# Performance work log

Hardware: AMD Instinct MI355X
Metric: run time of the kernel (lower is better)

The kernel has to match this reference:

```python
import jax, jax.numpy as jnp
import numpy as np

VOCAB = 32000
DIM = 1024
BATCH = 2
SEQ = 2048
CHUNK = 256
LCTX = 4            # local_context_size, mode='sum'
LOCAL_WIN = 512     # sparse_local_window (>= 2*chunk)
GSTRIDE = 1024      # sparse_global_stride (>= 4*chunk)
LN_EPS = 1e-5


def _cache_positions():
    """Simulate the deterministic sparse KV-cache pruning per chunk (numpy, trace-time).
    Returns list of key-position index arrays (cached positions ++ current chunk)."""
    cache = np.zeros((0,), dtype=np.int64)
    per_chunk = []
    for i in range(SEQ // CHUNK):
        new = np.arange(i * CHUNK, (i + 1) * CHUNK, dtype=np.int64)
        full = np.concatenate([cache, new])
        per_chunk.append(full)
        total_seen = (i + 1) * CHUNK
        local_start = max(0, total_seen - LOCAL_WIN)
        keep = (full >= local_start) | (full % GSTRIDE == 0)
        cache = full[keep]
    return per_chunk


def setup_inputs() -> dict:
    key = jax.random.key(0)
    ks = jax.random.split(key, 8)
    s = 0.02
    return {
        "x": jax.random.randint(ks[0], (BATCH, SEQ), 0, VOCAB, dtype=jnp.int64),
        "emb_table": jax.random.normal(ks[1], (VOCAB, DIM), jnp.float32) * s,
        "q_w": jax.random.normal(ks[2], (DIM, DIM), jnp.float32) * s,
        "q_b": jnp.zeros((DIM,), jnp.float32),
        "k_w": jax.random.normal(ks[3], (DIM, DIM), jnp.float32) * s,
        "k_b": jnp.zeros((DIM,), jnp.float32),
        "v_w": jax.random.normal(ks[4], (DIM, DIM), jnp.float32) * s,
        "v_b": jnp.zeros((DIM,), jnp.float32),
        "o_w": jax.random.normal(ks[5], (DIM, DIM), jnp.float32) * s,
        "o_b": jnp.zeros((DIM,), jnp.float32),
        "ln_w": jnp.ones((DIM,), jnp.float32),
        "ln_b": jnp.zeros((DIM,), jnp.float32),
        "out_w": jax.random.normal(ks[6], (VOCAB, DIM), jnp.float32) * s,
        "out_b": jnp.zeros((VOCAB,), jnp.float32),
    }


def reference(x, emb_table, q_w, q_b, k_w, k_b, v_w, v_b, o_w, o_b, ln_w, ln_b, out_w, out_b):
    # embedding + causal local context (sum of 0..LCTX-1 shifted embeddings)
    emb = emb_table[x]                                  # [B,S,D]
    ctx = emb
    for off in range(1, LCTX):
        ctx = ctx + jnp.pad(emb, ((0, 0), (off, 0), (0, 0)))[:, :SEQ]

    # project full sequence once (same per-chunk projections in the original)
    Q = ctx @ q_w.T + q_b                               # [B,S,D]
    K = ctx @ k_w.T + k_b
    V = ctx @ v_w.T + v_b
    scale = 1.0 / np.sqrt(DIM).astype(np.float32)

    outs = []
    for i, kpos in enumerate(_cache_positions()):
        qpos = np.arange(i * CHUNK, (i + 1) * CHUNK, dtype=np.int64)
        q = Q[:, i * CHUNK:(i + 1) * CHUNK]             # [B,C,D]
        k = K[:, kpos]                                  # [B,Ki,D] gathered sparse cache + chunk
        v = V[:, kpos]
        scores = jnp.einsum('bqd,bkd->bqk', q, k) * scale
        mask = kpos[None, :] > qpos[:, None]            # [C,Ki] static causal mask
        scores = jnp.where(mask[None, :, :], -jnp.inf, scores)
        w = jax.nn.softmax(scores, axis=-1)
        outs.append(jnp.einsum('bqk,bkd->bqd', w, v))

    attended = jnp.concatenate(outs, axis=1)            # [B,S,D]
    h = attended @ o_w.T + o_b
    # LayerNorm
    mu = h.mean(-1, keepdims=True)
    var = ((h - mu) ** 2).mean(-1, keepdims=True)
    h = (h - mu) / jnp.sqrt(var + LN_EPS) * ln_w + ln_b
    return h @ out_w.T + out_b                          # [B,S,VOCAB]
```

## Files before the change

### kernel.cpp

```cpp
#include <hip/hip_runtime.h>
#include <stdint.h>

#define DIMN 1024
#define SEQN 2048
#define BATCHN 2
#define NCHUNK 8
#define CHUNKSZ 256
#define VOCABN 32000
#define ROWS_PB 6016
#define PSTRIDE_B (256*ROWS_PB)
#define LN_EPS 1e-5f

#define MBIG 4096
#define NBIG 32000
#define KBIG 1024
#define NTILES_K (KBIG/64)

typedef unsigned short ushort_t;
typedef __attribute__((ext_vector_type(8))) __bf16 bf16x8;
typedef __attribute__((ext_vector_type(4))) float f32x4;

__device__ const int d_nk[8]   = {256,512,768,769,769,769,769,770};
__device__ const int d_np[8]   = {256,512,768,896,896,896,896,896};
__device__ const int d_koff[8] = {0,256,768,1536,2432,3328,4224,5120};

__device__ __forceinline__ ushort_t f2bu(float f) {
  union { float f; unsigned u; } v; v.f = f;
  unsigned r = v.u + 0x7FFFu + ((v.u >> 16) & 1u);
  return (ushort_t)(r >> 16);
}
__device__ __forceinline__ float b2f(ushort_t u) {
  union { unsigned u; float f; } v; v.u = ((unsigned)u) << 16; return v.f;
}

__device__ __forceinline__ int pos_of(int i, int j) {
  if (i <= 2) return j;
  if (i <= 6) return (j == 0) ? 0 : (i - 3) * 256 + 255 + j;
  return (j == 0) ? 0 : ((j == 1) ? 1024 : 1278 + j);
}

__device__ __forceinline__ void gload16(const void* g, void* l) {
  __builtin_amdgcn_global_load_lds((__attribute__((address_space(1))) void*)g,
                                   (__attribute__((address_space(3))) void*)l,
                                   16, 0, 0);
}

__device__ __forceinline__ void mma_core_s(const ushort_t* __restrict__ A,
                                           const ushort_t* __restrict__ Bt,
                                           int K, ushort_t* lA, ushort_t* lB,
                                           f32x4 acc[4][4], int tid) {
  const int lane = tid & 63;
  const int wr = (tid >> 7) & 1;
  const int wc = (tid >> 6) & 1;
  const int frow = lane & 15;
  const int lhi = lane >> 4;
  const int xk = (frow & 7) << 4;
  const size_t ldb = (size_t)K * 2;
  for (int kt = 0; kt < K; kt += 64) {
#pragma unroll
    for (int t = 0; t < 4; ++t) {
      int cid = t * 256 + tid;
      int row = cid >> 3;
      int srcoff = ((cid & 7) * 16) ^ ((row & 7) << 4);
      gload16((const char*)A  + (size_t)row * ldb + (size_t)kt * 2 + srcoff,
              (char*)lA + cid * 16);
      gload16((const char*)Bt + (size_t)row * ldb + (size_t)kt * 2 + srcoff,
              (char*)lB + cid * 16);
    }
    __syncthreads();
#pragma unroll
    for (int kk = 0; kk < 2; ++kk) {
      bf16x8 af[4], bfr[4];
#pragma unroll
      for (int m = 0; m < 4; ++m) {
        int r = wr * 64 + m * 16 + frow;
        af[m] = *(const bf16x8*)((const char*)lA +
                 ((r * 128 + kk * 64 + lhi * 16) ^ xk));
      }
#pragma unroll
      for (int n = 0; n < 4; ++n) {
        int r = wc * 64 + n * 16 + frow;
        bfr[n] = *(const bf16x8*)((const char*)lB +
                  ((r * 128 + kk * 64 + lhi * 16) ^ xk));
      }
#pragma unroll
      for (int m = 0; m < 4; ++m)
#pragma unroll
        for (int n = 0; n < 4; ++n)
          acc[m][n] = __builtin_amdgcn_mfma_f32_16x16x32_bf16(af[m], bfr[n],
                                                              acc[m][n], 0, 0, 0);
    }
    __syncthreads();
  }
}

__device__ __forceinline__ void stage_tile_big(const char* Abase, const char* Bbase,
                                               ushort_t* ldsbuf, int ktile, int tid) {
  const size_t ldb = (size_t)KBIG * 2;
#pragma unroll
  for (int s = 0; s < 4; ++s) {
    const char* base = (s < 2 ? Abase : Bbase) + (size_t)(s & 1) * 128 * ldb
                       + (size_t)ktile * 128;
    ushort_t* lh = ldsbuf + s * 8192;
#pragma unroll
    for (int r2 = 0; r2 < 2; ++r2) {
      int c = r2 * 512 + tid;
      int row = c >> 3;
      int off_l = (c * 16) ^ ((row & 7) << 4);
      gload16(base + (size_t)row * ldb + (off_l & 127), (char*)lh + c * 16);
    }
  }
}

__global__ __launch_bounds__(512, 2) void k_vocab(
    const ushort_t* __restrict__ A, const ushort_t* __restrict__ Bt,
    const float* __restrict__ bias, float* __restrict__ C) {
  __shared__ ushort_t lds[2][4][8192];
  const int tid = threadIdx.x;
  const int lane = tid & 63, w = tid >> 6, wm = w >> 2, wn = w & 3;
  const int frow = lane & 15, lhi = lane >> 4;
  const int xk = (frow & 7) << 4;

  int l = blockIdx.x;
  int swz = (l & 7) * ((int)gridDim.x >> 3) + (l >> 3);
  const int mt = swz & 15;
  const int nt = swz >> 4;
  const char* Abase = (const char*)(A + (size_t)mt * 256 * KBIG);
  const char* Bbase = (const char*)(Bt + (size_t)nt * 256 * KBIG);

  f32x4 acc[8][4] = {};

  stage_tile_big(Abase, Bbase, &lds[0][0][0], 0, tid);

  for (int kt = 0; kt < NTILES_K; ++kt) {
    const int cur = kt & 1;
    __builtin_amdgcn_sched_barrier(0);
    if (kt + 1 < NTILES_K) {
      stage_tile_big(Abase, Bbase, &lds[cur ^ 1][0][0], kt + 1, tid);
      asm volatile("s_waitcnt vmcnt(8)");
    } else {
      asm volatile("s_waitcnt vmcnt(0)");
    }
    __builtin_amdgcn_s_barrier();
    __builtin_amdgcn_sched_barrier(0);

    const char* lA = (const char*)&lds[cur][wm][0];
    const char* lB = (const char*)&lds[cur][2 + (wn >> 1)][0];

    bf16x8 bF[4][2];
#pragma unroll
    for (int fc = 0; fc < 4; ++fc) {
      int c = (wn & 1) * 64 + fc * 16 + frow;
#pragma unroll
      for (int kk = 0; kk < 2; ++kk)
        bF[fc][kk] = *(const bf16x8*)(lB + ((c * 128 + kk * 64 + lhi * 16) ^ xk));
    }
#pragma unroll
    for (int q = 0; q < 4; ++q) {
      bf16x8 aF[2][2];
#pragma unroll
      for (int i = 0; i < 2; ++i) {
        int r = (2 * q + i) * 16 + frow;
#pragma unroll
        for (int kk = 0; kk < 2; ++kk)
          aF[i][kk] = *(const bf16x8*)(lA + ((r * 128 + kk * 64 + lhi * 16) ^ xk));
      }
      if (q) __builtin_amdgcn_s_barrier();
      __builtin_amdgcn_s_setprio(1);
#pragma unroll
      for (int i = 0; i < 2; ++i)
#pragma unroll
        for (int fc = 0; fc < 4; ++fc)
#pragma unroll
          for (int kk = 0; kk < 2; ++kk)
            acc[2 * q + i][fc] = __builtin_amdgcn_mfma_f32_16x16x32_bf16(
                aF[i][kk], bF[fc][kk], acc[2 * q + i][fc], 0, 0, 0);
      __builtin_amdgcn_s_setprio(0);
    }
    __builtin_amdgcn_s_barrier();
  }

  const int rbase = mt * 256 + wm * 128 + lhi * 4;
  const int cbase = nt * 256 + wn * 64 + frow;
#pragma unroll
  for (int fc = 0; fc < 4; ++fc) {
    float bv = bias[cbase + fc * 16];
#pragma unroll
    for (int fr = 0; fr < 8; ++fr)
#pragma unroll
      for (int j = 0; j < 4; ++j)
        C[(size_t)(rbase + fr * 16 + j) * NBIG + cbase + fc * 16] =
            acc[fr][fc][j] + bv;
  }
}

#define SEG (DIMN*DIMN/4)
__global__ __launch_bounds__(256) void k_cvt5(
    const float* __restrict__ qw, const float* __restrict__ kw,
    const float* __restrict__ vw, const float* __restrict__ ow,
    const float* __restrict__ outw, ushort_t* __restrict__ wqkvb,
    ushort_t* __restrict__ wob, ushort_t* __restrict__ woutb) {
  const int total = 4 * SEG + (VOCABN * DIMN / 4);
  int idx = blockIdx.x * 256 + threadIdx.x;
  int stride = gridDim.x * 256;
  for (int i = idx; i < total; i += stride) {
    const float4* src; ushort4* dst;
    if (i < 3 * SEG) {
      src = (const float4*)(i < SEG ? qw : i < 2 * SEG ? kw : vw) +
            (i - (i < SEG ? 0 : i < 2 * SEG ? SEG : 2 * SEG));
      dst = (ushort4*)wqkvb + i;
    } else if (i < 4 * SEG) {
      src = (const float4*)ow + (i - 3 * SEG);
      dst = (ushort4*)wob + (i - 3 * SEG);
    } else {
      src = (const float4*)outw + (i - 4 * SEG);
      dst = (ushort4*)woutb + (i - 4 * SEG);
    }
    float4 v = *src;
    *dst = make_ushort4(f2bu(v.x), f2bu(v.y), f2bu(v.z), f2bu(v.w));
  }
}

__global__ __launch_bounds__(256) void k_embed(const int* __restrict__ x,
                                               const float* __restrict__ emb,
                                               ushort_t* __restrict__ ctxb) {
  const int t = blockIdx.x, b = blockIdx.y, tid = threadIdx.x;
  float4 s = make_float4(0.f, 0.f, 0.f, 0.f);
#pragma unroll
  for (int o = 0; o < 4; ++o) {
    if (t - o < 0) break;
    int tok = x[b * SEQN + t - o];
    float4 v = ((const float4*)(emb + (size_t)tok * DIMN))[tid];
    s.x += v.x; s.y += v.y; s.z += v.z; s.w += v.w;
  }
  ((ushort4*)(ctxb + ((size_t)(b * SEQN + t)) * DIMN))[tid] =
      make_ushort4(f2bu(s.x), f2bu(s.y), f2bu(s.z), f2bu(s.w));
}

__global__ __launch_bounds__(256) void k_qkv(const ushort_t* __restrict__ A,
    const ushort_t* __restrict__ Bt, const float* __restrict__ qb2,
    const float* __restrict__ kb2, const float* __restrict__ vb2,
    ushort_t* __restrict__ Qb, ushort_t* __restrict__ Kb,
    ushort_t* __restrict__ Vb) {
  int l = blockIdx.x;
  int swz = (l & 7) * ((int)gridDim.x >> 3) + (l >> 3);
  const int mt = swz & 31;
  const int nt = swz >> 5;
  __shared__ __align__(16) ushort_t lA[128*64];
  __shared__ __align__(16) ushort_t lB[128*64];
  f32x4 acc[4][4] = {};
  const int tid = threadIdx.x;
  mma_core_s(A + (size_t)mt * 128 * KBIG,
             Bt + (size_t)nt * 128 * KBIG, KBIG, lA, lB, acc, tid);
  const int which = nt >> 3;
  const int col0  = (nt & 7) * 128;
  ushort_t* Out = (which == 0) ? Qb : (which == 1) ? Kb : Vb;
  const float* Bv = (which == 0) ? qb2 : (which == 1) ? kb2 : vb2;
  const int lane = tid & 63, wr = (tid >> 7) & 1, wc = (tid >> 6) & 1;
  const int rbase = mt * 128 + wr * 64 + (lane >> 4) * 4;
  const int cbase = col0 + wc * 64 + (lane & 15);
#pragma unroll
  for (int m = 0; m < 4; ++m)
#pragma unroll
    for (int n = 0; n < 4; ++n) {
      int c = cbase + n * 16;
      float bv = Bv[c];
#pragma unroll
      for (int j = 0; j < 4; ++j)
        Out[(size_t)(rbase + m * 16 + j) * DIMN + c] = f2bu(acc[m][n][j] + bv);
    }
}

__global__ __launch_bounds__(256) void k_oproj(const ushort_t* __restrict__ A,
    const ushort_t* __restrict__ Bt, const float* __restrict__ bias,
    ushort_t* __restrict__ C) {
  __shared__ __align__(16) ushort_t lA[128*64];
  __shared__ __align__(16) ushort_t lB[128*64];
  f32x4 acc[4][4] = {};
  const int tid = threadIdx.x;
  mma_core_s(A + (size_t)blockIdx.y * 128 * KBIG,
             Bt + (size_t)blockIdx.x * 128 * KBIG, KBIG, lA, lB, acc, tid);
  const int lane = tid & 63, wr = (tid >> 7) & 1, wc = (tid >> 6) & 1;
  const int rbase = blockIdx.y * 128 + wr * 64 + (lane >> 4) * 4;
  const int cbase = blockIdx.x * 128 + wc * 64 + (lane & 15);
#pragma unroll
  for (int m = 0; m < 4; ++m)
#pragma unroll
    for (int n = 0; n < 4; ++n) {
      int c = cbase + n * 16;
      float bv = bias[c];
#pragma unroll
      for (int j = 0; j < 4; ++j)
        C[(size_t)(rbase + m * 16 + j) * DIMN + c] = f2bu(acc[m][n][j] + bv);
    }
}

__global__ __launch_bounds__(256) void k_gatherK(const ushort_t* __restrict__ Kb,
                                                 ushort_t* __restrict__ Kg) {
  const int r = blockIdx.x, b = blockIdx.y, tid = threadIdx.x;
  int i = 7;
#pragma unroll
  for (int q = 0; q < 7; ++q) if (r < d_koff[q + 1]) { i = q; break; }
  const int j = r - d_koff[i];
  ushort4* dst = (ushort4*)(Kg + ((size_t)b * ROWS_PB + r) * DIMN);
  if (j < d_nk[i]) {
    int pos = pos_of(i, j);
    dst[tid] = ((const ushort4*)(Kb + ((size_t)b * SEQN + pos) * DIMN))[tid];
  } else {
    dst[tid] = make_ushort4(0, 0, 0, 0);
  }
}

__global__ __launch_bounds__(256) void k_transV(const ushort_t* __restrict__ Vb,
                                                ushort_t* __restrict__ VgT) {
  __shared__ ushort_t tile[64][66];
  const int z = blockIdx.z, b = z >> 3, i = z & 7;
  const int np = d_np[i], nk = d_nk[i], ko = d_koff[i];
  const int jb = blockIdx.x * 64;
  if (jb >= np) return;
  const int db = blockIdx.y * 64;
  const int tid = threadIdx.x, tx = tid & 63, ty = tid >> 6;
#pragma unroll
  for (int rep = 0; rep < 16; ++rep) {
    int jl = rep * 4 + ty;
    int j = jb + jl;
    ushort_t v = 0;
    if (j < nk) v = Vb[((size_t)b * SEQN + pos_of(i, j)) * DIMN + db + tx];
    tile[jl][tx] = v;
  }
  __syncthreads();
  const size_t base = ((size_t)b * ROWS_PB + ko) * DIMN;
#pragma unroll
  for (int rep = 0; rep < 16; ++rep) {
    int dl = rep * 4 + ty;
    VgT[base + (size_t)(db + dl) * np + jb + tx] = tile[tx][dl];
  }
}

__global__ __launch_bounds__(256) void k_scores(const ushort_t* __restrict__ Qb,
    const ushort_t* __restrict__ Kg, ushort_t* __restrict__ P) {
  const int z = blockIdx.z, b = z >> 3, i = z & 7;
  const int np = d_np[i], nk = d_nk[i], ko = d_koff[i];
  if ((int)blockIdx.x * 128 >= np) return;
  __shared__ __align__(16) ushort_t lA[128*64];
  __shared__ __align__(16) ushort_t lB[128*64];
  f32x4 acc[4][4] = {};
  const int tid = threadIdx.x;
  const ushort_t* A  = Qb + ((size_t)(b * SEQN + i * CHUNKSZ) + blockIdx.y * 128) * DIMN;
  const ushort_t* Bt = Kg + ((size_t)b * ROWS_PB + ko + blockIdx.x * 128) * DIMN;
  mma_core_s(A, Bt, DIMN, lA, lB, acc, tid);
  const int lane = tid & 63, wr = (tid >> 7) & 1, wc = (tid >> 6) & 1;
  const int rb = blockIdx.y * 128 + wr * 64 + (lane >> 4) * 4;
  const int cb = blockIdx.x * 128 + wc * 64 + (lane & 15);
  ushort_t* Pc = P + (size_t)b * PSTRIDE_B + (size_t)ko * 256;
  const float scale = 0.03125f;
  const int diag0 = nk - CHUNKSZ;
#pragma unroll
  for (int m = 0; m < 4; ++m)
#pragma unroll
    for (int n = 0; n < 4; ++n) {
      int c = cb + n * 16;
#pragma unroll
      for (int j = 0; j < 4; ++j) {
        int r = rb + m * 16 + j;
        float w = 0.0f;
        if (c < nk && (c - diag0) <= r) w = expf(acc[m][n][j] * scale);
        Pc[(size_t)r * np + c] = f2bu(w);
      }
    }
}

__global__ __launch_bounds__(256) void k_rowsum(const ushort_t* __restrict__ P,
                                                float* __restrict__ rowsum) {
  const int z = blockIdx.y, b = z >> 3, i = z & 7, r = blockIdx.x;
  const int np = d_np[i], ko = d_koff[i];
  const ushort_t* row = P + (size_t)b * PSTRIDE_B + (size_t)ko * 256 + (size_t)r * np;
  const int tid = threadIdx.x;
  float s = 0.f;
  for (int c = tid; c < np; c += 256) s += b2f(row[c]);
#pragma unroll
  for (int o = 1; o < 64; o <<= 1) s += __shfl_xor(s, o);
  __shared__ float ss[4];
  if ((tid & 63) == 0) ss[tid >> 6] = s;
  __syncthreads();
  if (tid == 0) rowsum[z * 256 + r] = ss[0] + ss[1] + ss[2] + ss[3];
}

__global__ __launch_bounds__(256) void k_pv(const ushort_t* __restrict__ P,
    const ushort_t* __restrict__ VgT, const float* __restrict__ rowsum,
    ushort_t* __restrict__ attb) {
  const int z = blockIdx.z, b = z >> 3, i = z & 7;
  const int np = d_np[i], ko = d_koff[i];
  __shared__ __align__(16) ushort_t lA[128*64];
  __shared__ __align__(16) ushort_t lB[128*64];
  f32x4 acc[4][4] = {};
  const int tid = threadIdx.x;
  const ushort_t* A  = P + (size_t)b * PSTRIDE_B + (size_t)ko * 256 +
                       (size_t)blockIdx.y * 128 * np;
  const ushort_t* Bt = VgT + ((size_t)b * ROWS_PB + ko) * DIMN +
                       (size_t)blockIdx.x * 128 * np;
  mma_core_s(A, Bt, np, lA, lB, acc, tid);
  const int lane = tid & 63, wr = (tid >> 7) & 1, wc = (tid >> 6) & 1;
  const int rb = blockIdx.y * 128 + wr * 64 + (lane >> 4) * 4;
  const int cb = blockIdx.x * 128 + wc * 64 + (lane & 15);
  const float* rs = rowsum + z * 256;
  ushort_t* outp = attb + (size_t)(b * SEQN + i * CHUNKSZ) * DIMN;
#pragma unroll
  for (int m = 0; m < 4; ++m)
#pragma unroll
    for (int j = 0; j < 4; ++j) {
      int r = rb + m * 16 + j;
      float inv = 1.0f / rs[r];
#pragma unroll
      for (int n = 0; n < 4; ++n)
        outp[(size_t)r * DIMN + cb + n * 16] = f2bu(acc[m][n][j] * inv);
    }
}

__global__ __launch_bounds__(256) void k_ln(const ushort_t* __restrict__ h,
    const float* __restrict__ lnw, const float* __restrict__ lnb,
    ushort_t* __restrict__ hb) {
  const int row = blockIdx.x, tid = threadIdx.x;
  ushort4 u4 = ((const ushort4*)(h + (size_t)row * DIMN))[tid];
  float4 v = make_float4(b2f(u4.x), b2f(u4.y), b2f(u4.z), b2f(u4.w));
  float s  = v.x + v.y + v.z + v.w;
  float sq = v.x * v.x + v.y * v.y + v.z * v.z + v.w * v.w;
#pragma unroll
  for (int o = 1; o < 64; o <<= 1) { s += __shfl_xor(s, o); sq += __shfl_xor(sq, o); }
  __shared__ float ss[4], ssq[4];
  if ((tid & 63) == 0) { ss[tid >> 6] = s; ssq[tid >> 6] = sq; }
  __syncthreads();
  s  = ss[0] + ss[1] + ss[2] + ss[3];
  sq = ssq[0] + ssq[1] + ssq[2] + ssq[3];
  const float mu  = s * (1.0f / DIMN);
  const float var = sq * (1.0f / DIMN) - mu * mu;
  const float inv = rsqrtf(var + LN_EPS);
  float4 w4 = ((const float4*)lnw)[tid];
  float4 b4 = ((const float4*)lnb)[tid];
  ushort4 o4 = make_ushort4(f2bu((v.x - mu) * inv * w4.x + b4.x),
                            f2bu((v.y - mu) * inv * w4.y + b4.y),
                            f2bu((v.z - mu) * inv * w4.z + b4.z),
                            f2bu((v.w - mu) * inv * w4.w + b4.w));
  ((ushort4*)(hb + (size_t)row * DIMN))[tid] = o4;
}

extern "C" void kernel_launch(void* const* d_in, const int* in_sizes, int n_in,
                              void* d_out, int out_size, void* d_ws, size_t ws_size,
                              hipStream_t stream) {
  const int*   x    = (const int*)  d_in[0];
  const float* emb  = (const float*)d_in[1];
  const float* qw   = (const float*)d_in[2];
  const float* qb   = (const float*)d_in[3];
  const float* kw   = (const float*)d_in[4];
  const float* kb   = (const float*)d_in[5];
  const float* vw   = (const float*)d_in[6];
  const float* vb   = (const float*)d_in[7];
  const float* ow   = (const float*)d_in[8];
  const float* ob   = (const float*)d_in[9];
  const float* lnw  = (const float*)d_in[10];
  const float* lnb  = (const float*)d_in[11];
  const float* outw = (const float*)d_in[12];
  const float* outb = (const float*)d_in[13];
  float* out = (float*)d_out;
  (void)in_sizes; (void)n_in; (void)out_size; (void)ws_size;

  char* ws = (char*)d_ws;
  size_t off = 0;
  auto alloc = [&](size_t bytes) {
    size_t r = off; off += (bytes + 255) & ~(size_t)255; return r;
  };
  ushort_t* wqkvb = (ushort_t*)(ws + alloc((size_t)3 * DIMN * DIMN * 2));
  ushort_t* wob   = (ushort_t*)(ws + alloc((size_t)DIMN * DIMN * 2));
  ushort_t* woutb = (ushort_t*)(ws + alloc((size_t)VOCABN * DIMN * 2));
  ushort_t* ctxb  = (ushort_t*)(ws + alloc((size_t)BATCHN * SEQN * DIMN * 2));
  ushort_t* Qb    = (ushort_t*)(ws + alloc((size_t)BATCHN * SEQN * DIMN * 2));
  ushort_t* Kb    = (ushort_t*)(ws + alloc((size_t)BATCHN * SEQN * DIMN * 2));
  ushort_t* Vb    = (ushort_t*)(ws + alloc((size_t)BATCHN * SEQN * DIMN * 2));
  ushort_t* Kg    = (ushort_t*)(ws + alloc((size_t)BATCHN * ROWS_PB * DIMN * 2));
  ushort_t* VgT   = (ushort_t*)(ws + alloc((size_t)BATCHN * ROWS_PB * DIMN * 2));
  ushort_t* Pm    = (ushort_t*)(ws + alloc((size_t)BATCHN * PSTRIDE_B * 2));
  float*    rsum  = (float*)   (ws + alloc((size_t)BATCHN * NCHUNK * 256 * 4));
  ushort_t* attb  = (ushort_t*)(ws + alloc((size_t)BATCHN * SEQN * DIMN * 2));
  ushort_t* hbuf  = (ushort_t*)(ws + alloc((size_t)BATCHN * SEQN * DIMN * 2));
  ushort_t* hb    = (ushort_t*)(ws + alloc((size_t)BATCHN * SEQN * DIMN * 2));

  k_cvt5<<<dim3(4096), dim3(256), 0, stream>>>(qw, kw, vw, ow, outw,
                                               wqkvb, wob, woutb);

  k_embed<<<dim3(SEQN, BATCHN), dim3(256), 0, stream>>>(x, emb, ctxb);

  k_qkv<<<dim3(768), dim3(256), 0, stream>>>(ctxb, wqkvb, qb, kb, vb,
                                             Qb, Kb, Vb);

  k_gatherK<<<dim3(ROWS_PB, BATCHN), dim3(256), 0, stream>>>(Kb, Kg);
  k_transV<<<dim3(14, 16, BATCHN * NCHUNK), dim3(256), 0, stream>>>(Vb, VgT);

  k_scores<<<dim3(7, 2, BATCHN * NCHUNK), dim3(256), 0, stream>>>(Qb, Kg, Pm);
  k_rowsum<<<dim3(256, BATCHN * NCHUNK), dim3(256), 0, stream>>>(Pm, rsum);
  k_pv<<<dim3(8, 2, BATCHN * NCHUNK), dim3(256), 0, stream>>>(Pm, VgT, rsum, attb);

  k_oproj<<<dim3(8, 32), dim3(256), 0, stream>>>(attb, wob, ob, hbuf);
  k_ln<<<dim3(BATCHN * SEQN), dim3(256), 0, stream>>>(hbuf, lnw, lnb, hb);

  k_vocab<<<dim3(2000), dim3(512), 0, stream>>>(hb, woutb, outb, out);
}
```

Measured before the change: 589.2 us.

## Fuse K gather into scores GEMM loads and use nontemporal vocab stores

Removes the separate K-gather kernel and its materialized gathered-K buffer. The scores kernel instead computes per-row source addresses from the sparse cache position map and loads K rows directly from the projected K buffer inside its own tiled MFMA loop. The vocab GEMM output stores become nontemporal to avoid polluting cache with the large logits write. The inlined score loop is a simpler single-buffered version that may pipeline less well than the shared core routine.

```diff
diff --git a/kernel.cpp b/kernel.cpp
--- a/kernel.cpp
+++ b/kernel.cpp
@@ -189,8 +189,8 @@
     for (int fr = 0; fr < 8; ++fr)
 #pragma unroll
       for (int j = 0; j < 4; ++j)
-        C[(size_t)(rbase + fr * 16 + j) * NBIG + cbase + fc * 16] =
-            acc[fr][fc][j] + bv;
+        __builtin_nontemporal_store(acc[fr][fc][j] + bv,
+            &C[(size_t)(rbase + fr * 16 + j) * NBIG + cbase + fc * 16]);
   }
 }
 
@@ -295,22 +295,6 @@
     }
 }
 
-__global__ __launch_bounds__(256) void k_gatherK(const ushort_t* __restrict__ Kb,
-                                                 ushort_t* __restrict__ Kg) {
-  const int r = blockIdx.x, b = blockIdx.y, tid = threadIdx.x;
-  int i = 7;
-#pragma unroll
-  for (int q = 0; q < 7; ++q) if (r < d_koff[q + 1]) { i = q; break; }
-  const int j = r - d_koff[i];
-  ushort4* dst = (ushort4*)(Kg + ((size_t)b * ROWS_PB + r) * DIMN);
-  if (j < d_nk[i]) {
-    int pos = pos_of(i, j);
-    dst[tid] = ((const ushort4*)(Kb + ((size_t)b * SEQN + pos) * DIMN))[tid];
-  } else {
-    dst[tid] = make_ushort4(0, 0, 0, 0);
-  }
-}
-
 __global__ __launch_bounds__(256) void k_transV(const ushort_t* __restrict__ Vb,
                                                 ushort_t* __restrict__ VgT) {
   __shared__ ushort_t tile[64][66];
@@ -338,7 +322,7 @@
 }
 
 __global__ __launch_bounds__(256) void k_scores(const ushort_t* __restrict__ Qb,
-    const ushort_t* __restrict__ Kg, ushort_t* __restrict__ P) {
+    const ushort_t* __restrict__ Kb, ushort_t* __restrict__ P) {
   const int z = blockIdx.z, b = z >> 3, i = z & 7;
   const int np = d_np[i], nk = d_nk[i], ko = d_koff[i];
   if ((int)blockIdx.x * 128 >= np) return;
@@ -346,10 +330,59 @@
   __shared__ __align__(16) ushort_t lB[128*64];
   f32x4 acc[4][4] = {};
   const int tid = threadIdx.x;
-  const ushort_t* A  = Qb + ((size_t)(b * SEQN + i * CHUNKSZ) + blockIdx.y * 128) * DIMN;
-  const ushort_t* Bt = Kg + ((size_t)b * ROWS_PB + ko + blockIdx.x * 128) * DIMN;
-  mma_core_s(A, Bt, DIMN, lA, lB, acc, tid);
   const int lane = tid & 63, wr = (tid >> 7) & 1, wc = (tid >> 6) & 1;
+  const int frow = lane & 15, lhi = lane >> 4;
+  const int xk = (frow & 7) << 4;
+
+  const char* sA[4]; const char* sB[4];
+  {
+    const char* Aq = (const char*)(Qb +
+        ((size_t)(b * SEQN + i * CHUNKSZ) + blockIdx.y * 128) * DIMN);
+#pragma unroll
+    for (int t = 0; t < 4; ++t) {
+      int cid = t * 256 + tid;
+      int row = cid >> 3;
+      int srcoff = ((cid & 7) * 16) ^ ((row & 7) << 4);
+      sA[t] = Aq + (size_t)row * 2048 + srcoff;
+      int jg = blockIdx.x * 128 + row;
+      int pos = (jg < nk) ? pos_of(i, jg) : 0;
+      sB[t] = (const char*)(Kb + ((size_t)b * SEQN + pos) * DIMN) + srcoff;
+    }
+  }
+
+  for (int kt = 0; kt < KBIG; kt += 64) {
+#pragma unroll
+    for (int t = 0; t < 4; ++t) {
+      int cid = t * 256 + tid;
+      gload16(sA[t] + (size_t)kt * 2, (char*)lA + cid * 16);
+      gload16(sB[t] + (size_t)kt * 2, (char*)lB + cid * 16);
+    }
+    __syncthreads();
+#pragma unroll
+    for (int kk = 0; kk < 2; ++kk) {
+      bf16x8 af[4], bfr[4];
+#pragma unroll
+      for (int m = 0; m < 4; ++m) {
+        int r = wr * 64 + m * 16 + frow;
+        af[m] = *(const bf16x8*)((const char*)lA +
+                 ((r * 128 + kk * 64 + lhi * 16) ^ xk));
+      }
+#pragma unroll
+      for (int n = 0; n < 4; ++n) {
+        int r = wc * 64 + n * 16 + frow;
+        bfr[n] = *(const bf16x8*)((const char*)lB +
+                  ((r * 128 + kk * 64 + lhi * 16) ^ xk));
+      }
+#pragma unroll
+      for (int m = 0; m < 4; ++m)
+#pragma unroll
+        for (int n = 0; n < 4; ++n)
+          acc[m][n] = __builtin_amdgcn_mfma_f32_16x16x32_bf16(af[m], bfr[n],
+                                                              acc[m][n], 0, 0, 0);
+    }
+    __syncthreads();
+  }
+
   const int rb = blockIdx.y * 128 + wr * 64 + (lane >> 4) * 4;
   const int cb = blockIdx.x * 128 + wc * 64 + (lane & 15);
   ushort_t* Pc = P + (size_t)b * PSTRIDE_B + (size_t)ko * 256;
@@ -476,7 +509,6 @@
   ushort_t* Qb    = (ushort_t*)(ws + alloc((size_t)BATCHN * SEQN * DIMN * 2));
   ushort_t* Kb    = (ushort_t*)(ws + alloc((size_t)BATCHN * SEQN * DIMN * 2));
   ushort_t* Vb    = (ushort_t*)(ws + alloc((size_t)BATCHN * SEQN * DIMN * 2));
-  ushort_t* Kg    = (ushort_t*)(ws + alloc((size_t)BATCHN * ROWS_PB * DIMN * 2));
   ushort_t* VgT   = (ushort_t*)(ws + alloc((size_t)BATCHN * ROWS_PB * DIMN * 2));
   ushort_t* Pm    = (ushort_t*)(ws + alloc((size_t)BATCHN * PSTRIDE_B * 2));
   float*    rsum  = (float*)   (ws + alloc((size_t)BATCHN * NCHUNK * 256 * 4));
@@ -492,10 +524,9 @@
   k_qkv<<<dim3(768), dim3(256), 0, stream>>>(ctxb, wqkvb, qb, kb, vb,
                                              Qb, Kb, Vb);
 
-  k_gatherK<<<dim3(ROWS_PB, BATCHN), dim3(256), 0, stream>>>(Kb, Kg);
   k_transV<<<dim3(14, 16, BATCHN * NCHUNK), dim3(256), 0, stream>>>(Vb, VgT);
 
-  k_scores<<<dim3(7, 2, BATCHN * NCHUNK), dim3(256), 0, stream>>>(Qb, Kg, Pm);
+  k_scores<<<dim3(7, 2, BATCHN * NCHUNK), dim3(256), 0, stream>>>(Qb, Kb, Pm);
   k_rowsum<<<dim3(256, BATCHN * NCHUNK), dim3(256), 0, stream>>>(Pm, rsum);
   k_pv<<<dim3(8, 2, BATCHN * NCHUNK), dim3(256), 0, stream>>>(Pm, VgT, rsum, attb);
 
```

After: 520.6 us. 11.6% less time.
